# Kernel tuning notes

Hardware: AMD Instinct MI355X
Metric: run time of the kernel (lower is better)

Reference implementation:

```python
import jax, jax.numpy as jnp
import numpy as np

N_PEDS = 4096
GRID_N = 16          # grid is GRID_N x GRID_N cells
CELL_SIDE = 0.6      # meters per cell
POOL_DIM = 2         # DIRECTIONAL pooling: relative (vx, vy)
OUT_DIM = 256
H_DIM = 128
AREA = 20.0          # scene is AREA x AREA meters


def setup_inputs() -> dict:
    key = jax.random.key(0)
    k1, k2, k3, k4, k5 = jax.random.split(key, 5)
    positions = jax.random.uniform(k1, (N_PEDS, 2), dtype=jnp.float32) * AREA
    # past position = current minus a small per-step displacement (~pedestrian velocity)
    past_positions = positions - jax.random.normal(k2, (N_PEDS, 2), dtype=jnp.float32) * 0.4
    h = jax.random.normal(k3, (N_PEDS, H_DIM), dtype=jnp.float32)
    in_dim = GRID_N * GRID_N * POOL_DIM
    scale = 1.0 / np.sqrt(in_dim)
    W_emb = jax.random.uniform(k4, (OUT_DIM, in_dim), dtype=jnp.float32, minval=-scale, maxval=scale)
    b_emb = jax.random.uniform(k5, (OUT_DIM,), dtype=jnp.float32, minval=-scale, maxval=scale)
    return {"h": h, "positions": positions, "past_positions": past_positions,
            "W_emb": W_emb, "b_emb": b_emb}


def _directional_grid(positions, past_positions):
    """DIRECTIONAL grid pooling: bin neighbours' relative velocities into an
    n x n grid (cell_side meters per cell) centred on each pedestrian, averaging
    contributions per cell (norm_cell=True). Returns [N, n*n, 2]."""
    n = GRID_N
    num = positions.shape[0]
    vel = positions - past_positions                         # [N, 2]
    rel_pos = positions[None, :, :] - positions[:, None, :]  # [N, N, 2] pos_j - pos_i
    rel_vel = vel[None, :, :] - vel[:, None, :]              # [N, N, 2] vel_j - vel_i
    # cell indices: floor(rel/cell + n/2)
    oij = jnp.floor(rel_pos / CELL_SIDE + n / 2).astype(jnp.int32)  # [N, N, 2]
    in_range = jnp.all((oij >= 0) & (oij < n), axis=-1)             # [N, N]
    valid = in_range & ~jnp.eye(num, dtype=bool)                    # exclude self
    cell_idx = jnp.where(valid, oij[..., 0] * n + oij[..., 1], 0)   # [N, N]
    vals = jnp.where(valid[..., None], rel_vel, 0.0)                # [N, N, 2]
    rows = jnp.arange(num)[:, None]                                 # [N, 1]
    grid = jnp.zeros((num, n * n, POOL_DIM), dtype=positions.dtype)
    grid = grid.at[rows, cell_idx].add(vals)                        # scatter-add values
    cnt = jnp.zeros((num, n * n), dtype=positions.dtype)
    cnt = cnt.at[rows, cell_idx].add(valid.astype(positions.dtype)) # occupancy counts
    grid = grid / jnp.maximum(cnt, 1.0)[..., None]                  # norm_cell: mean per cell
    return grid


def reference(h, positions, past_positions, W_emb, b_emb):
    grid = _directional_grid(positions, past_positions)      # [N, n*n, 2]
    flat = grid.reshape(grid.shape[0], -1)                   # [N, n*n*2]
    return jax.nn.relu(flat @ W_emb.T + b_emb)               # [N, out_dim]
```

## Files before the change

kernel.cpp:

```cpp
#include <hip/hip_runtime.h>

typedef __attribute__((ext_vector_type(4))) float f32x4;
typedef __attribute__((ext_vector_type(8))) short bf16x8;

#define NP 4096
#define IB 2

__device__ __forceinline__ unsigned short f2bf(float f) {
  unsigned int u = __float_as_uint(f);
  u = u + 0x7FFFu + ((u >> 16) & 1u);
  return (unsigned short)(u >> 16);
}

__global__ __launch_bounds__(256, 8) void pool_kernel(
    const float2* __restrict__ pos, const float2* __restrict__ past,
    unsigned short* __restrict__ gridws) {
  __shared__ unsigned long long acc[IB][256];
  const int tid = threadIdx.x;
  const int tx = tid & (IB - 1);
  const int ty = tid >> 1;
  const int ibase = blockIdx.x * IB;
  const int i = ibase + tx;

  for (int idx = tid; idx < IB * 256 * 2; idx += 256)
    ((unsigned int*)acc)[idx] = 0u;
  __syncthreads();

  const float2 pi = pos[i];
  const float2 qi = past[i];
  const float vix = pi.x - qi.x;
  const float viy = pi.y - qi.y;
  unsigned long long* accp = acc[tx];
  const float inv06 = 1.0f / 0.6f;

  auto process = [&](float2 pj, float2 qj) {
    float rx = pj.x - pi.x;
    float ry = pj.y - pi.y;
    float ax = __builtin_fmaf(rx, inv06, 8.0f);
    float ay = __builtin_fmaf(ry, inv06, 8.0f);
    bool unc = (fabsf(ax - rintf(ax)) < 1e-4f) |
               (fabsf(ay - rintf(ay)) < 1e-4f);
    float fx, fy;
    if (__any(unc)) {
      fx = floorf(rx / 0.6f + 8.0f);
      fy = floorf(ry / 0.6f + 8.0f);
    } else {
      fx = floorf(ax);
      fy = floorf(ay);
    }
    int ix = (int)fx;
    int iy = (int)fy;
    if (((unsigned)ix < 16u) & ((unsigned)iy < 16u)) {
      float rvx = (pj.x - qj.x) - vix;
      float rvy = (pj.y - qj.y) - viy;
      unsigned int qx = (unsigned int)((int)rintf(rvx * 2048.0f) + 16384);
      unsigned int qy = (unsigned int)((int)rintf(rvy * 2048.0f) + 16384);
      unsigned long long p = ((unsigned long long)qx << 38) |
                             ((unsigned long long)qy << 12) | 1ull;
      atomicAdd(&accp[(ix << 4) + iy], p);
    }
  };

  for (int jo = 0; jo < NP; jo += 512) {
    int j0 = jo + ty;
    float2 p0 = pos[j0];        float2 q0 = past[j0];
    float2 p1 = pos[j0 + 128];  float2 q1 = past[j0 + 128];
    float2 p2 = pos[j0 + 256];  float2 q2 = past[j0 + 256];
    float2 p3 = pos[j0 + 384];  float2 q3 = past[j0 + 384];
    process(p0, q0);
    process(p1, q1);
    process(p2, q2);
    process(p3, q3);
  }
  __syncthreads();

  const int cell = tid;
  const float selfc = (cell == 136) ? 1.0f : 0.0f;
#pragma unroll
  for (int il = 0; il < IB; ++il) {
    unsigned long long raw = acc[il][cell];
    unsigned int cnt = (unsigned int)(raw & 0xFFFull);
    int sxq = (int)((unsigned int)(raw >> 38)) - (int)(cnt << 14);
    int syq = (int)((unsigned int)((raw >> 12) & 0x3FFFFFFull)) - (int)(cnt << 14);
    float cn = (float)cnt - selfc;
    float d = fmaxf(cn, 1.0f);
    float sx = (float)sxq * (1.0f / 2048.0f);
    float sy = (float)syq * (1.0f / 2048.0f);
    unsigned int packed =
        ((unsigned int)f2bf(sy / d) << 16) | (unsigned int)f2bf(sx / d);
    *(unsigned int*)&gridws[(size_t)(ibase + il) * 512 + cell * 2] = packed;
  }
}

__global__ __launch_bounds__(256) void wconv_kernel(
    const float* __restrict__ W, unsigned short* __restrict__ Wb) {
  int i = (blockIdx.x * 256 + threadIdx.x) * 8;
  float4 w0 = *(const float4*)&W[i];
  float4 w1 = *(const float4*)&W[i + 4];
  bf16x8 bv;
  bv[0] = (short)f2bf(w0.x); bv[1] = (short)f2bf(w0.y);
  bv[2] = (short)f2bf(w0.z); bv[3] = (short)f2bf(w0.w);
  bv[4] = (short)f2bf(w1.x); bv[5] = (short)f2bf(w1.y);
  bv[6] = (short)f2bf(w1.z); bv[7] = (short)f2bf(w1.w);
  *(bf16x8*)&Wb[i] = bv;
}

__global__ __launch_bounds__(128) void gemm_kernel(
    const unsigned short* __restrict__ A, const unsigned short* __restrict__ Wb,
    const float* __restrict__ bias, float* __restrict__ out) {
  const int lane = threadIdx.x & 63;
  const int w = threadIdx.x >> 6;
  const int mbase = blockIdx.y * 64 + w * 32;
  const int nbase = blockIdx.x * 64;
  const int lrow = lane & 15;
  const int lk = (lane >> 4) * 8;

  f32x4 acc[2][4] = {};

  for (int kb = 0; kb < 512; kb += 64) {
    bf16x8 a[2][2], b[2][4];
#pragma unroll
    for (int ks = 0; ks < 2; ++ks) {
      const int k0 = kb + ks * 32 + lk;
#pragma unroll
      for (int mf = 0; mf < 2; ++mf)
        a[ks][mf] = *(const bf16x8*)&A[(size_t)(mbase + mf * 16 + lrow) * 512 + k0];
#pragma unroll
      for (int nf = 0; nf < 4; ++nf)
        b[ks][nf] = *(const bf16x8*)&Wb[(size_t)(nbase + nf * 16 + lrow) * 512 + k0];
    }
#pragma unroll
    for (int ks = 0; ks < 2; ++ks)
#pragma unroll
      for (int mf = 0; mf < 2; ++mf)
#pragma unroll
        for (int nf = 0; nf < 4; ++nf)
          acc[mf][nf] = __builtin_amdgcn_mfma_f32_16x16x32_bf16(
              a[ks][mf], b[ks][nf], acc[mf][nf], 0, 0, 0);
  }

  const int rq = (lane >> 4) * 4;
#pragma unroll
  for (int nf = 0; nf < 4; ++nf) {
    const int col = nbase + nf * 16 + lrow;
    const float bv = bias[col];
#pragma unroll
    for (int mf = 0; mf < 2; ++mf) {
      const int row0 = mbase + mf * 16 + rq;
#pragma unroll
      for (int q = 0; q < 4; ++q) {
        float v = acc[mf][nf][q] + bv;
        out[(size_t)(row0 + q) * 256 + col] = fmaxf(v, 0.0f);
      }
    }
  }
}

extern "C" void kernel_launch(void* const* d_in, const int* in_sizes, int n_in,
                              void* d_out, int out_size, void* d_ws, size_t ws_size,
                              hipStream_t stream) {
  const float2* pos = (const float2*)d_in[1];
  const float2* past = (const float2*)d_in[2];
  const float* W = (const float*)d_in[3];
  const float* bias = (const float*)d_in[4];
  float* out = (float*)d_out;

  unsigned short* gridws = (unsigned short*)d_ws;
  unsigned short* Wb = (unsigned short*)((char*)d_ws + 4 * 1024 * 1024);

  wconv_kernel<<<(256 * 512) / (256 * 8), 256, 0, stream>>>(W, Wb);
  pool_kernel<<<NP / IB, 256, 0, stream>>>(pos, past, gridws);
  dim3 g(256 / 64, NP / 64);
  gemm_kernel<<<g, 128, 0, stream>>>(gridws, Wb, bias, out);
}
```

Measured before the change: 41.20 us.

## Pack pooling accumulators into 32-bit LDS atomics and stage GEMM tiles in LDS

The pooling kernel now packs count and both relative-velocity sums into a single 32-bit word, not a 64-bit one, so it can use 32-bit shared-memory atomics. Velocity quantisation drops from 1/2048 to 1/64, and the fields shrink to a 6-bit count and 13-bit sums. This makes the atomics cheaper but risks overflow in crowded cells and adds rounding error. The GEMM is also restructured into 256-thread blocks covering 32 rows, with register-prefetched global loads staged through padded LDS tiles.

```diff
diff --git a/kernel.cpp b/kernel.cpp
--- a/kernel.cpp
+++ b/kernel.cpp
@@ -15,22 +15,21 @@
 __global__ __launch_bounds__(256, 8) void pool_kernel(
     const float2* __restrict__ pos, const float2* __restrict__ past,
     unsigned short* __restrict__ gridws) {
-  __shared__ unsigned long long acc[IB][256];
+  __shared__ unsigned int acc[IB][256];
   const int tid = threadIdx.x;
   const int tx = tid & (IB - 1);
   const int ty = tid >> 1;
   const int ibase = blockIdx.x * IB;
   const int i = ibase + tx;
 
-  for (int idx = tid; idx < IB * 256 * 2; idx += 256)
-    ((unsigned int*)acc)[idx] = 0u;
+  for (int idx = tid; idx < IB * 256; idx += 256) ((unsigned int*)acc)[idx] = 0u;
   __syncthreads();
 
   const float2 pi = pos[i];
   const float2 qi = past[i];
   const float vix = pi.x - qi.x;
   const float viy = pi.y - qi.y;
-  unsigned long long* accp = acc[tx];
+  unsigned int* accp = acc[tx];
   const float inv06 = 1.0f / 0.6f;
 
   auto process = [&](float2 pj, float2 qj) {
@@ -53,10 +52,10 @@
     if (((unsigned)ix < 16u) & ((unsigned)iy < 16u)) {
       float rvx = (pj.x - qj.x) - vix;
       float rvy = (pj.y - qj.y) - viy;
-      unsigned int qx = (unsigned int)((int)rintf(rvx * 2048.0f) + 16384);
-      unsigned int qy = (unsigned int)((int)rintf(rvy * 2048.0f) + 16384);
-      unsigned long long p = ((unsigned long long)qx << 38) |
-                             ((unsigned long long)qy << 12) | 1ull;
+      int qx = (int)rintf(rvx * 64.0f);
+      int qy = (int)rintf(rvy * 64.0f);
+      unsigned int p = ((unsigned int)(qx + 256) << 19) |
+                       ((unsigned int)(qy + 256) << 6) | 1u;
       atomicAdd(&accp[(ix << 4) + iy], p);
     }
   };
@@ -78,14 +77,14 @@
   const float selfc = (cell == 136) ? 1.0f : 0.0f;
 #pragma unroll
   for (int il = 0; il < IB; ++il) {
-    unsigned long long raw = acc[il][cell];
-    unsigned int cnt = (unsigned int)(raw & 0xFFFull);
-    int sxq = (int)((unsigned int)(raw >> 38)) - (int)(cnt << 14);
-    int syq = (int)((unsigned int)((raw >> 12) & 0x3FFFFFFull)) - (int)(cnt << 14);
+    unsigned int raw = acc[il][cell];
+    unsigned int cnt = raw & 63u;
+    int sxq = (int)(raw >> 19) - (int)(cnt << 8);
+    int syq = (int)((raw >> 6) & 0x1FFFu) - (int)(cnt << 8);
     float cn = (float)cnt - selfc;
     float d = fmaxf(cn, 1.0f);
-    float sx = (float)sxq * (1.0f / 2048.0f);
-    float sy = (float)syq * (1.0f / 2048.0f);
+    float sx = (float)sxq * (1.0f / 64.0f);
+    float sy = (float)syq * (1.0f / 64.0f);
     unsigned int packed =
         ((unsigned int)f2bf(sy / d) << 16) | (unsigned int)f2bf(sx / d);
     *(unsigned int*)&gridws[(size_t)(ibase + il) * 512 + cell * 2] = packed;
@@ -105,53 +104,66 @@
   *(bf16x8*)&Wb[i] = bv;
 }
 
-__global__ __launch_bounds__(128) void gemm_kernel(
+__global__ __launch_bounds__(256) void gemm_kernel(
     const unsigned short* __restrict__ A, const unsigned short* __restrict__ Wb,
     const float* __restrict__ bias, float* __restrict__ out) {
-  const int lane = threadIdx.x & 63;
-  const int w = threadIdx.x >> 6;
-  const int mbase = blockIdx.y * 64 + w * 32;
+  __shared__ unsigned short As[32][72];
+  __shared__ unsigned short Bs[64][72];
+  const int tid = threadIdx.x;
+  const int lane = tid & 63;
+  const int w = tid >> 6;
+  const int mf = w & 1;
+  const int nc = w >> 1;
+  const int mbase = blockIdx.y * 32;
   const int nbase = blockIdx.x * 64;
   const int lrow = lane & 15;
   const int lk = (lane >> 4) * 8;
 
-  f32x4 acc[2][4] = {};
+  const int ar = tid >> 3;
+  const int ac = (tid & 7) * 8;
+  const int br = tid >> 2;
+  const int bc = (tid & 3) * 16;
 
-  for (int kb = 0; kb < 512; kb += 64) {
-    bf16x8 a[2][2], b[2][4];
+  f32x4 acc[2] = {};
+
+  const unsigned short* Arow = &A[(size_t)(mbase + ar) * 512 + ac];
+  const unsigned short* Brow = &Wb[(size_t)(nbase + br) * 512 + bc];
+
+  bf16x8 ra = *(const bf16x8*)Arow;
+  bf16x8 rb0 = *(const bf16x8*)Brow;
+  bf16x8 rb1 = *(const bf16x8*)(Brow + 8);
+
+  for (int step = 0; step < 8; ++step) {
+    *(bf16x8*)&As[ar][ac] = ra;
+    *(bf16x8*)&Bs[br][bc] = rb0;
+    *(bf16x8*)&Bs[br][bc + 8] = rb1;
+    __syncthreads();
+    if (step < 7) {
+      ra = *(const bf16x8*)(Arow + (step + 1) * 64);
+      rb0 = *(const bf16x8*)(Brow + (step + 1) * 64);
+      rb1 = *(const bf16x8*)(Brow + (step + 1) * 64 + 8);
+    }
 #pragma unroll
     for (int ks = 0; ks < 2; ++ks) {
-      const int k0 = kb + ks * 32 + lk;
-#pragma unroll
-      for (int mf = 0; mf < 2; ++mf)
-        a[ks][mf] = *(const bf16x8*)&A[(size_t)(mbase + mf * 16 + lrow) * 512 + k0];
-#pragma unroll
-      for (int nf = 0; nf < 4; ++nf)
-        b[ks][nf] = *(const bf16x8*)&Wb[(size_t)(nbase + nf * 16 + lrow) * 512 + k0];
+      bf16x8 a = *(const bf16x8*)&As[mf * 16 + lrow][ks * 32 + lk];
+      bf16x8 b0 = *(const bf16x8*)&Bs[nc * 32 + lrow][ks * 32 + lk];
+      bf16x8 b1 = *(const bf16x8*)&Bs[nc * 32 + 16 + lrow][ks * 32 + lk];
+      acc[0] = __builtin_amdgcn_mfma_f32_16x16x32_bf16(a, b0, acc[0], 0, 0, 0);
+      acc[1] = __builtin_amdgcn_mfma_f32_16x16x32_bf16(a, b1, acc[1], 0, 0, 0);
     }
-#pragma unroll
-    for (int ks = 0; ks < 2; ++ks)
-#pragma unroll
-      for (int mf = 0; mf < 2; ++mf)
-#pragma unroll
-        for (int nf = 0; nf < 4; ++nf)
-          acc[mf][nf] = __builtin_amdgcn_mfma_f32_16x16x32_bf16(
-              a[ks][mf], b[ks][nf], acc[mf][nf], 0, 0, 0);
+    __syncthreads();
   }
 
   const int rq = (lane >> 4) * 4;
+  const int row0 = mbase + mf * 16 + rq;
 #pragma unroll
-  for (int nf = 0; nf < 4; ++nf) {
-    const int col = nbase + nf * 16 + lrow;
+  for (int nf = 0; nf < 2; ++nf) {
+    const int col = nbase + (nc * 2 + nf) * 16 + lrow;
     const float bv = bias[col];
 #pragma unroll
-    for (int mf = 0; mf < 2; ++mf) {
-      const int row0 = mbase + mf * 16 + rq;
-#pragma unroll
-      for (int q = 0; q < 4; ++q) {
-        float v = acc[mf][nf][q] + bv;
-        out[(size_t)(row0 + q) * 256 + col] = fmaxf(v, 0.0f);
-      }
+    for (int q = 0; q < 4; ++q) {
+      float v = acc[nf][q] + bv;
+      out[(size_t)(row0 + q) * 256 + col] = fmaxf(v, 0.0f);
     }
   }
 }
@@ -170,6 +182,6 @@
 
   wconv_kernel<<<(256 * 512) / (256 * 8), 256, 0, stream>>>(W, Wb);
   pool_kernel<<<NP / IB, 256, 0, stream>>>(pos, past, gridws);
-  dim3 g(256 / 64, NP / 64);
-  gemm_kernel<<<g, 128, 0, stream>>>(gridws, Wb, bias, out);
+  dim3 g(256 / 64, NP / 32);
+  gemm_kernel<<<g, 256, 0, stream>>>(gridws, Wb, bias, out);
 }
```

Measured after the change: 36.75 us. 10.8% less time.

## Fuse grid pooling and embedding GEMM into one kernel with 16 pedestrians per block

Applied to the files above, without the earlier changes.

Merges the pooling kernel and the GEMM kernel. Each 512-thread block now bins neighbours for 16 pedestrians, keeps the bf16 grid in shared memory, and runs the MFMA GEMM against the bf16 weights directly. This removes the global round trip of the 4 MB intermediate grid and one kernel launch, and each block reads pos/past once for 16 pedestrians instead of 2. In exchange the grid has only 256 blocks, each block re-reads the full 256 KB of weights from L2, and the 32 KB of shared atomics per block may limit occupancy.

```diff
diff --git a/kernel.cpp b/kernel.cpp
--- a/kernel.cpp
+++ b/kernel.cpp
@@ -4,7 +4,8 @@
 typedef __attribute__((ext_vector_type(8))) short bf16x8;
 
 #define NP 4096
-#define IB 2
+#define IB 16
+#define GP 520
 
 __device__ __forceinline__ unsigned short f2bf(float f) {
   unsigned int u = __float_as_uint(f);
@@ -12,18 +13,33 @@
   return (unsigned short)(u >> 16);
 }
 
-__global__ __launch_bounds__(256, 8) void pool_kernel(
+__global__ __launch_bounds__(256) void wconv_kernel(
+    const float* __restrict__ W, unsigned short* __restrict__ Wb) {
+  int i = (blockIdx.x * 256 + threadIdx.x) * 8;
+  float4 w0 = *(const float4*)&W[i];
+  float4 w1 = *(const float4*)&W[i + 4];
+  bf16x8 bv;
+  bv[0] = (short)f2bf(w0.x); bv[1] = (short)f2bf(w0.y);
+  bv[2] = (short)f2bf(w0.z); bv[3] = (short)f2bf(w0.w);
+  bv[4] = (short)f2bf(w1.x); bv[5] = (short)f2bf(w1.y);
+  bv[6] = (short)f2bf(w1.z); bv[7] = (short)f2bf(w1.w);
+  *(bf16x8*)&Wb[i] = bv;
+}
+
+__global__ __launch_bounds__(512) void fused_kernel(
     const float2* __restrict__ pos, const float2* __restrict__ past,
-    unsigned short* __restrict__ gridws) {
+    const unsigned short* __restrict__ Wb, const float* __restrict__ bias,
+    float* __restrict__ out) {
   __shared__ unsigned long long acc[IB][256];
+  __shared__ unsigned short grid[IB][GP];
   const int tid = threadIdx.x;
-  const int tx = tid & (IB - 1);
-  const int ty = tid >> 1;
+  const int tx = tid & 15;
+  const int ty = tid >> 4;
   const int ibase = blockIdx.x * IB;
   const int i = ibase + tx;
 
-  for (int idx = tid; idx < IB * 256 * 2; idx += 256)
-    ((unsigned int*)acc)[idx] = 0u;
+  for (int idx = tid; idx < IB * 256; idx += 512)
+    acc[idx >> 8][idx & 255] = 0ull;
   __syncthreads();
 
   const float2 pi = pos[i];
@@ -61,12 +77,12 @@
     }
   };
 
-  for (int jo = 0; jo < NP; jo += 512) {
+  for (int jo = 0; jo < NP; jo += 128) {
     int j0 = jo + ty;
-    float2 p0 = pos[j0];        float2 q0 = past[j0];
-    float2 p1 = pos[j0 + 128];  float2 q1 = past[j0 + 128];
-    float2 p2 = pos[j0 + 256];  float2 q2 = past[j0 + 256];
-    float2 p3 = pos[j0 + 384];  float2 q3 = past[j0 + 384];
+    float2 p0 = pos[j0];       float2 q0 = past[j0];
+    float2 p1 = pos[j0 + 32];  float2 q1 = past[j0 + 32];
+    float2 p2 = pos[j0 + 64];  float2 q2 = past[j0 + 64];
+    float2 p3 = pos[j0 + 96];  float2 q3 = past[j0 + 96];
     process(p0, q0);
     process(p1, q1);
     process(p2, q2);
@@ -74,85 +90,57 @@
   }
   __syncthreads();
 
-  const int cell = tid;
-  const float selfc = (cell == 136) ? 1.0f : 0.0f;
 #pragma unroll
-  for (int il = 0; il < IB; ++il) {
-    unsigned long long raw = acc[il][cell];
+  for (int idx = tid; idx < IB * 256; idx += 512) {
+    const int ped = idx >> 8;
+    const int cell = idx & 255;
+    unsigned long long raw = acc[ped][cell];
     unsigned int cnt = (unsigned int)(raw & 0xFFFull);
     int sxq = (int)((unsigned int)(raw >> 38)) - (int)(cnt << 14);
     int syq = (int)((unsigned int)((raw >> 12) & 0x3FFFFFFull)) - (int)(cnt << 14);
-    float cn = (float)cnt - selfc;
+    float cn = (float)cnt - ((cell == 136) ? 1.0f : 0.0f);
     float d = fmaxf(cn, 1.0f);
     float sx = (float)sxq * (1.0f / 2048.0f);
     float sy = (float)syq * (1.0f / 2048.0f);
     unsigned int packed =
         ((unsigned int)f2bf(sy / d) << 16) | (unsigned int)f2bf(sx / d);
-    *(unsigned int*)&gridws[(size_t)(ibase + il) * 512 + cell * 2] = packed;
+    *(unsigned int*)&grid[ped][cell * 2] = packed;
   }
-}
+  __syncthreads();
 
-__global__ __launch_bounds__(256) void wconv_kernel(
-    const float* __restrict__ W, unsigned short* __restrict__ Wb) {
-  int i = (blockIdx.x * 256 + threadIdx.x) * 8;
-  float4 w0 = *(const float4*)&W[i];
-  float4 w1 = *(const float4*)&W[i + 4];
-  bf16x8 bv;
-  bv[0] = (short)f2bf(w0.x); bv[1] = (short)f2bf(w0.y);
-  bv[2] = (short)f2bf(w0.z); bv[3] = (short)f2bf(w0.w);
-  bv[4] = (short)f2bf(w1.x); bv[5] = (short)f2bf(w1.y);
-  bv[6] = (short)f2bf(w1.z); bv[7] = (short)f2bf(w1.w);
-  *(bf16x8*)&Wb[i] = bv;
-}
+  const int lane = tid & 63;
+  const int w = tid >> 6;
+  const int lrow = lane & 15;
+  const int lk8 = (lane >> 4) * 8;
+  const int nb = w * 32;
 
-__global__ __launch_bounds__(128) void gemm_kernel(
-    const unsigned short* __restrict__ A, const unsigned short* __restrict__ Wb,
-    const float* __restrict__ bias, float* __restrict__ out) {
-  const int lane = threadIdx.x & 63;
-  const int w = threadIdx.x >> 6;
-  const int mbase = blockIdx.y * 64 + w * 32;
-  const int nbase = blockIdx.x * 64;
-  const int lrow = lane & 15;
-  const int lk = (lane >> 4) * 8;
+  f32x4 o0 = {0.f, 0.f, 0.f, 0.f};
+  f32x4 o1 = {0.f, 0.f, 0.f, 0.f};
 
-  f32x4 acc[2][4] = {};
-
-  for (int kb = 0; kb < 512; kb += 64) {
-    bf16x8 a[2][2], b[2][4];
+  for (int ks = 0; ks < 16; ks += 4) {
+    bf16x8 av[4], b0[4], b1[4];
 #pragma unroll
-    for (int ks = 0; ks < 2; ++ks) {
-      const int k0 = kb + ks * 32 + lk;
-#pragma unroll
-      for (int mf = 0; mf < 2; ++mf)
-        a[ks][mf] = *(const bf16x8*)&A[(size_t)(mbase + mf * 16 + lrow) * 512 + k0];
-#pragma unroll
-      for (int nf = 0; nf < 4; ++nf)
-        b[ks][nf] = *(const bf16x8*)&Wb[(size_t)(nbase + nf * 16 + lrow) * 512 + k0];
+    for (int u = 0; u < 4; ++u) {
+      const int k0 = (ks + u) * 32 + lk8;
+      av[u] = *(const bf16x8*)&grid[lrow][k0];
+      b0[u] = *(const bf16x8*)&Wb[(size_t)(nb + lrow) * 512 + k0];
+      b1[u] = *(const bf16x8*)&Wb[(size_t)(nb + 16 + lrow) * 512 + k0];
     }
 #pragma unroll
-    for (int ks = 0; ks < 2; ++ks)
-#pragma unroll
-      for (int mf = 0; mf < 2; ++mf)
-#pragma unroll
-        for (int nf = 0; nf < 4; ++nf)
-          acc[mf][nf] = __builtin_amdgcn_mfma_f32_16x16x32_bf16(
-              a[ks][mf], b[ks][nf], acc[mf][nf], 0, 0, 0);
+    for (int u = 0; u < 4; ++u) {
+      o0 = __builtin_amdgcn_mfma_f32_16x16x32_bf16(av[u], b0[u], o0, 0, 0, 0);
+      o1 = __builtin_amdgcn_mfma_f32_16x16x32_bf16(av[u], b1[u], o1, 0, 0, 0);
+    }
   }
 
   const int rq = (lane >> 4) * 4;
+  const float bv0 = bias[nb + lrow];
+  const float bv1 = bias[nb + 16 + lrow];
 #pragma unroll
-  for (int nf = 0; nf < 4; ++nf) {
-    const int col = nbase + nf * 16 + lrow;
-    const float bv = bias[col];
-#pragma unroll
-    for (int mf = 0; mf < 2; ++mf) {
-      const int row0 = mbase + mf * 16 + rq;
-#pragma unroll
-      for (int q = 0; q < 4; ++q) {
-        float v = acc[mf][nf][q] + bv;
-        out[(size_t)(row0 + q) * 256 + col] = fmaxf(v, 0.0f);
-      }
-    }
+  for (int q = 0; q < 4; ++q) {
+    const size_t row = (size_t)(ibase + rq + q) * 256;
+    out[row + nb + lrow] = fmaxf(o0[q] + bv0, 0.0f);
+    out[row + nb + 16 + lrow] = fmaxf(o1[q] + bv1, 0.0f);
   }
 }
 
@@ -165,11 +153,8 @@
   const float* bias = (const float*)d_in[4];
   float* out = (float*)d_out;
 
-  unsigned short* gridws = (unsigned short*)d_ws;
-  unsigned short* Wb = (unsigned short*)((char*)d_ws + 4 * 1024 * 1024);
+  unsigned short* Wb = (unsigned short*)d_ws;
 
   wconv_kernel<<<(256 * 512) / (256 * 8), 256, 0, stream>>>(W, Wb);
-  pool_kernel<<<NP / IB, 256, 0, stream>>>(pos, past, gridws);
-  dim3 g(256 / 64, NP / 64);
-  gemm_kernel<<<g, 128, 0, stream>>>(gridws, Wb, bias, out);
+  fused_kernel<<<NP / IB, 512, 0, stream>>>(pos, past, Wb, bias, out);
 }
```

Measured after the change: 43.36 us. 5.2% more time.
